# Performance work log

Measured on AMD Instinct MI355X. Metric: run time of the kernel, lower is better.

The kernel has to match this reference:

```python
import jax, jax.numpy as jnp
import numpy as np
import math

EPS = 1e-5


def _layernorm(x, gamma, beta):
    mu = jnp.mean(x, axis=-1, keepdims=True)
    var = jnp.var(x, axis=-1, keepdims=True)
    return (x - mu) * jax.lax.rsqrt(var + EPS) * gamma + beta


def _quantum_head(x, theta_rx):
    # RX(x_i) then RX(theta_i) on wire i == RX(x_i + theta_i); product state,
    # CNOT ring is a Z-basis permutation => <Z_j> = prod_{i in S_j} cos(a_i)
    # with S_j = {0..j} for j>=1 (chain of CNOT(i,i+1)) and S_0 = {1..7}
    # (final CNOT(7,0) makes b0 = b1^...^b7).
    c = jnp.cos(x + theta_rx)                       # (B,S,8)
    cp = jnp.cumprod(c, axis=-1)                    # prefix products c0..cj
    z0 = jnp.prod(c[..., 1:], axis=-1, keepdims=True)
    return jnp.concatenate([z0, cp[..., 1:]], axis=-1)  # (B,S,8)


def _quantum_ffn(x, theta_ry):
    # RX(x_i) |0>, then RY(theta_i), measure Z: <Z_i> = cos(theta_i) * cos(x_i)
    return jnp.cos(theta_ry) * jnp.cos(x)


def setup_inputs() -> dict:
    key = jax.random.key(0)
    ks = jax.random.split(key, 6)
    B, S, E, F = 16, 2048, 8, 512
    return {
        'x': jax.random.normal(ks[0], (B, S, E), jnp.float32),
        'theta_rx': jax.random.normal(ks[1], (E,), jnp.float32),
        'w_out': jax.random.normal(ks[2], (E, E), jnp.float32) / math.sqrt(E),
        'theta_ry': jax.random.normal(ks[3], (E,), jnp.float32),
        'w1': jax.random.normal(ks[4], (F, E), jnp.float32) / math.sqrt(E),
        'b1': jnp.zeros((F,), jnp.float32),
        'w2': jax.random.normal(ks[5], (E, F), jnp.float32) / math.sqrt(F),
        'b2': jnp.zeros((E,), jnp.float32),
        'gamma1': jnp.ones((E,), jnp.float32),
        'beta1': jnp.zeros((E,), jnp.float32),
        'gamma2': jnp.ones((E,), jnp.float32),
        'beta2': jnp.zeros((E,), jnp.float32),
    }


def reference(x, theta_rx, w_out, theta_ry, w1, b1, w2, b2,
              gamma1, beta1, gamma2, beta2):
    B, S, E = x.shape
    H = 2
    D = E // H
    # --- quantum multi-head attention (shared head => q == k == v) ---
    z = _quantum_head(x, theta_rx)                       # (B,S,E)
    qh = z.reshape(B, S, H, D).transpose(0, 2, 1, 3)     # (B,H,S,D)
    scores = jnp.einsum('bhqd,bhkd->bhqk', qh, qh) / math.sqrt(D)
    attn = jax.nn.softmax(scores, axis=-1)
    out = jnp.einsum('bhqk,bhkd->bhqd', attn, qh)        # (B,H,S,D)
    out = out.transpose(0, 2, 1, 3).reshape(B, S, E)
    attn_out = out @ w_out.T                             # out_proj, no bias
    x1 = _layernorm(x + attn_out, gamma1, beta1)
    # --- quantum feed-forward ---
    zf = _quantum_ffn(x1, theta_ry)                      # (B,S,E)
    h = zf @ w1.T + b1                                   # (B,S,F)
    ffn_out = jax.nn.relu(h) @ w2.T + b2                 # (B,S,E)
    return _layernorm(x1 + ffn_out, gamma2, beta2)
```

## Files before the change

### kernel.cpp

```cpp
#include <hip/hip_runtime.h>
#include <math.h>
#include <utility>

#define NB 16
#define NS 2048
#define NE 8
#define NH 2
#define NF 512
#define DEG 6
#define NMONO 210
#define KPB 64
#define NCHUNK 32
#define PHI_LD 66
#define QPB 128
#define LNEPS 1e-5f
#define PART_STRIDE (5 * NMONO)

typedef float f32x2 __attribute__((ext_vector_type(2)));
typedef _Float16 h2 __attribute__((ext_vector_type(2)));

#if defined(__has_builtin)
# if __has_builtin(__builtin_amdgcn_fdot2)
#  define FDOT2(a,b,c) __builtin_amdgcn_fdot2((a),(b),(c),false)
# endif
#endif
#ifndef FDOT2
static __device__ __forceinline__ float fdot2_sw(h2 a, h2 b, float c) {
    return c + (float)a.x * (float)b.x + (float)a.y * (float)b.y;
}
# define FDOT2(a,b,c) fdot2_sw((a),(b),(c))
#endif

constexpr float ACOEF_C[7] = {0.99994459f, 2.00308514f, 2.00174650f,
                              1.30890404f, 0.65803033f, 0.31441604f, 0.10241921f};

constexpr int mono_e(int idx) {
    int i = 0;
    for (int e0 = 0; e0 <= DEG; ++e0)
        for (int e1 = 0; e1 <= DEG - e0; ++e1)
            for (int e2 = 0; e2 <= DEG - e0 - e1; ++e2)
                for (int e3 = 0; e3 <= DEG - e0 - e1 - e2; ++e3) {
                    if (i == idx) return (e0 << 12) | (e1 << 8) | (e2 << 4) | e3;
                    ++i;
                }
    return 0;
}
constexpr float mfact(int n) { float r = 1.f; for (int i = 2; i <= n; ++i) r *= (float)i; return r; }
constexpr float mono_c(int idx) {
    const int E = mono_e(idx);
    const int e0 = E >> 12, e1 = (E >> 8) & 15, e2 = (E >> 4) & 15, e3 = E & 15;
    const int d = e0 + e1 + e2 + e3;
    return ACOEF_C[d] * (mfact(d) / (mfact(e0) * mfact(e1) * mfact(e2) * mfact(e3)));
}

template <int BEG, class F, int... Is>
__device__ __forceinline__ void sf_impl(F f, std::integer_sequence<int, Is...>) {
    (f(std::integral_constant<int, BEG + Is>{}), ...);
}
template <int BEG, int END, class F>
__device__ __forceinline__ void static_for(F f) {
    sf_impl<BEG>(f, std::make_integer_sequence<int, END - BEG>{});
}

template <int BEG, int END>
__device__ __forceinline__ void phi_body(_Float16* __restrict__ Phi, int lane,
                                         const float (&pw0)[7], const float (&pw1)[7],
                                         const float (&pw2)[7], const float (&pw3)[7]) {
    static_for<BEG, END>([&](auto Ic) {
        constexpr int idx = Ic.value;
        constexpr int E = mono_e(idx);
        constexpr float C = mono_c(idx);
        const float v = C * (pw0[E >> 12] * pw1[(E >> 8) & 15]) *
                            (pw2[(E >> 4) & 15] * pw3[E & 15]);
        Phi[idx * PHI_LD + lane] = (_Float16)v;
    });
}

__global__ __launch_bounds__(256, 4)
void k1_moments(const float* __restrict__ x, const float* __restrict__ theta_rx,
                float* __restrict__ ws) {
    __shared__ _Float16 Phi[NMONO * PHI_LD];
    __shared__ __align__(16) _Float16 kvh[KPB / 2][8];
    __shared__ float th_s[8];

    const int t = threadIdx.x, bid = blockIdx.x;
    const int kc = bid & 31, h = (bid >> 5) & 1, b = bid >> 6;

    if (t < 8) th_s[t] = theta_rx[t];
    __syncthreads();

    const int lane = t & 63, wq = t >> 6;
    {
        const float* xr = x + ((size_t)b * NS + kc * KPB + lane) * NE;
        const float4 v0 = *reinterpret_cast<const float4*>(xr);
        const float4 v1 = *reinterpret_cast<const float4*>(xr + 4);
        const float c0 = __cosf(v0.x + th_s[0]), c1 = __cosf(v0.y + th_s[1]);
        const float c2 = __cosf(v0.z + th_s[2]), c3 = __cosf(v0.w + th_s[3]);
        const float c4 = __cosf(v1.x + th_s[4]), c5 = __cosf(v1.y + th_s[5]);
        const float c6 = __cosf(v1.z + th_s[6]), c7 = __cosf(v1.w + th_s[7]);
        const float p1 = c0*c1, p2 = p1*c2, p3 = p2*c3, p4 = p3*c4;
        const float p5 = p4*c5, p6 = p5*c6, p7 = p6*c7;
        float k0, k1v, k2v, k3v;
        if (h == 0) {
            const float s6 = c7*c6, s5 = s6*c5, s4 = s5*c4, s3 = s4*c3, s2 = s3*c2;
            k0 = s2*c1; k1v = p1; k2v = p2; k3v = p3;
        } else {
            k0 = p4; k1v = p5; k2v = p6; k3v = p7;
        }
        if (t < 64) {
            const int j = t >> 1, par = t & 1;
            kvh[j][0 + par] = (_Float16)k0;  kvh[j][2 + par] = (_Float16)k1v;
            kvh[j][4 + par] = (_Float16)k2v; kvh[j][6 + par] = (_Float16)k3v;
        }
        float pw0[7], pw1[7], pw2[7], pw3[7];
        pw0[0] = pw1[0] = pw2[0] = pw3[0] = 1.f;
        #pragma unroll
        for (int i = 1; i <= DEG; ++i) {
            pw0[i] = pw0[i-1] * k0;  pw1[i] = pw1[i-1] * k1v;
            pw2[i] = pw2[i-1] * k2v; pw3[i] = pw3[i-1] * k3v;
        }
        switch (wq) {
            case 0: phi_body<0,   53 >(Phi, lane, pw0, pw1, pw2, pw3); break;
            case 1: phi_body<53,  106>(Phi, lane, pw0, pw1, pw2, pw3); break;
            case 2: phi_body<106, 159>(Phi, lane, pw0, pw1, pw2, pw3); break;
            default: phi_body<159, 210>(Phi, lane, pw0, pw1, pw2, pw3); break;
        }
    }
    __syncthreads();

    if (t < NMONO) {
        const h2 one2 = {(_Float16)1.f, (_Float16)1.f};
        float a0 = 0.f, a1 = 0.f, a2 = 0.f, a3 = 0.f, a4 = 0.f;
        #pragma unroll 8
        for (int j = 0; j < KPB / 2; ++j) {
            const h2 phi2 = *reinterpret_cast<const h2*>(&Phi[t * PHI_LD + 2 * j]);
            const float4 kv4 = *reinterpret_cast<const float4*>(&kvh[j][0]);
            const h2 kA = __builtin_bit_cast(h2, kv4.x);
            const h2 kB = __builtin_bit_cast(h2, kv4.y);
            const h2 kC = __builtin_bit_cast(h2, kv4.z);
            const h2 kD = __builtin_bit_cast(h2, kv4.w);
            a0 = FDOT2(phi2, kA, a0);
            a1 = FDOT2(phi2, kB, a1);
            a2 = FDOT2(phi2, kC, a2);
            a3 = FDOT2(phi2, kD, a3);
            a4 = FDOT2(phi2, one2, a4);
        }
        float* dst = ws + (size_t)bid * PART_STRIDE;
        dst[0 * NMONO + t] = a0;
        dst[1 * NMONO + t] = a1;
        dst[2 * NMONO + t] = a2;
        dst[3 * NMONO + t] = a3;
        dst[4 * NMONO + t] = a4;
    }
}

template <int BEG, int END>
__device__ __forceinline__ void p2_body1(const float4* __restrict__ Mn,
                                         const float* __restrict__ Md, int base,
                                         const float (&pw)[4][7],
                                         f32x2& a01, f32x2& a23, float& ad) {
    static_for<BEG, END>([&](auto Ic) {
        constexpr int idx = Ic.value;
        constexpr int E = mono_e(idx);
        constexpr int e0 = E >> 12, e1 = (E >> 8) & 15, e2 = (E >> 4) & 15, e3 = E & 15;
        const float4 mv = Mn[base + idx];
        const float  md = Md[base + idx];
        const float P = (pw[0][e0] * pw[1][e1]) * (pw[2][e2] * pw[3][e3]);
        a01 += P * (f32x2){mv.x, mv.y};
        a23 += P * (f32x2){mv.z, mv.w};
        ad  += P * md;
    });
}

__global__ __launch_bounds__(1024, 4)
void k2_main(const float* __restrict__ x, const float* __restrict__ theta_rx,
             const float* __restrict__ w_out, const float* __restrict__ theta_ry,
             const float* __restrict__ w1, const float* __restrict__ b1,
             const float* __restrict__ w2, const float* __restrict__ b2,
             const float* __restrict__ g1, const float* __restrict__ be1,
             const float* __restrict__ g2, const float* __restrict__ be2,
             const float* __restrict__ ws, float* __restrict__ out) {
    __shared__ float4 Mn_lds[2 * NMONO];
    __shared__ float  Md_lds[2 * NMONO];
    __shared__ float  z_c[8][QPB];
    __shared__ float  x1_c[8][QPB];
    __shared__ float  zf_c[8][QPB];
    __shared__ float  attn_c[8][QPB];
    __shared__ float  part_a[4][256][5];
    __shared__ float  w1_s[NF][NE];
    __shared__ float  w2t_s[NF][NE];
    __shared__ float  b1_s[NF];
    __shared__ float  wout_s[NE][NE];
    __shared__ float  th_s[8], cry_s[8], g1_s[8], be1_s[8], g2_s[8], be2_s[8], b2_s[8];

    const int t = threadIdx.x, bid = blockIdx.x;
    const int b  = (bid & 7) + 8 * ((bid >> 3) & 1);
    const int qc = bid >> 4;

    if (t < 2 * NMONO) {
        const int h = (t >= NMONO) ? 1 : 0;
        const int a = t - h * NMONO;
        const float* src = ws + (size_t)((b * 2 + h) * NCHUNK) * PART_STRIDE;
        float s0 = 0.f, s1 = 0.f, s2 = 0.f, s3 = 0.f, s4 = 0.f;
        #pragma unroll 4
        for (int kc = 0; kc < NCHUNK; ++kc) {
            const float* p = src + (size_t)kc * PART_STRIDE;
            s0 += p[0 * NMONO + a]; s1 += p[1 * NMONO + a];
            s2 += p[2 * NMONO + a]; s3 += p[3 * NMONO + a];
            s4 += p[4 * NMONO + a];
        }
        Mn_lds[t] = make_float4(s0, s1, s2, s3);
        Md_lds[t] = s4;
    }

    for (int i = t; i < NF * NE; i += 1024) {
        ((float*)w1_s)[i] = w1[i];
        const int e = i >> 9, f = i & (NF - 1);
        w2t_s[f][e] = w2[i];
    }
    if (t < NF) b1_s[t] = b1[t];
    if (t < NE * NE) ((float*)wout_s)[t] = w_out[t];
    if (t < 8) {
        th_s[t]  = theta_rx[t];
        cry_s[t] = __cosf(theta_ry[t]);
        g1_s[t]  = g1[t];  be1_s[t] = be1[t];
        g2_s[t]  = g2[t];  be2_s[t] = be2[t];
        b2_s[t]  = b2[t];
    }
    __syncthreads();

    if (t < QPB) {
        const float* xr = x + ((size_t)b * NS + qc * QPB + t) * NE;
        const float4 v0 = *reinterpret_cast<const float4*>(xr);
        const float4 v1 = *reinterpret_cast<const float4*>(xr + 4);
        const float c0 = __cosf(v0.x + th_s[0]), c1 = __cosf(v0.y + th_s[1]);
        const float c2 = __cosf(v0.z + th_s[2]), c3 = __cosf(v0.w + th_s[3]);
        const float c4 = __cosf(v1.x + th_s[4]), c5 = __cosf(v1.y + th_s[5]);
        const float c6 = __cosf(v1.z + th_s[6]), c7 = __cosf(v1.w + th_s[7]);
        const float p1 = c0*c1, p2 = p1*c2, p3 = p2*c3, p4 = p3*c4;
        const float p5 = p4*c5, p6 = p5*c6, p7 = p6*c7;
        const float s6 = c7*c6, s5 = s6*c5, s4 = s5*c4, s3 = s4*c3, s2 = s3*c2;
        z_c[0][t] = s2*c1; z_c[1][t] = p1; z_c[2][t] = p2; z_c[3][t] = p3;
        z_c[4][t] = p4;    z_c[5][t] = p5; z_c[6][t] = p6; z_c[7][t] = p7;
    }
    __syncthreads();

    {
        const int w = t >> 6, lane = t & 63;
        const int g = w & 3;
        const int h = (w >> 3) & 1;
        const int r = ((w >> 2) & 1) * 64 + lane;
        float pw[4][7];
        #pragma unroll
        for (int d = 0; d < 4; ++d) {
            const float u = z_c[h*4+d][r] * 0.25f;
            pw[d][0] = 1.f;
            #pragma unroll
            for (int i = 1; i <= DEG; ++i) pw[d][i] = pw[d][i-1] * u;
        }
        f32x2 a01 = {0.f,0.f}, a23 = {0.f,0.f};
        float ad = 0.f;
        const int base = h * NMONO;
        switch (g) {
            case 0: p2_body1<0,   53 >(Mn_lds, Md_lds, base, pw, a01, a23, ad); break;
            case 1: p2_body1<53,  106>(Mn_lds, Md_lds, base, pw, a01, a23, ad); break;
            case 2: p2_body1<106, 159>(Mn_lds, Md_lds, base, pw, a01, a23, ad); break;
            default: p2_body1<159, 210>(Mn_lds, Md_lds, base, pw, a01, a23, ad); break;
        }
        float* pa = &part_a[g][h * 128 + r][0];
        pa[0] = a01.x; pa[1] = a01.y; pa[2] = a23.x; pa[3] = a23.y; pa[4] = ad;
    }
    __syncthreads();

    if (t < 256) {
        const int h = t >> 7, r = t & 127;
        float n0 = 0.f, n1 = 0.f, n2 = 0.f, n3 = 0.f, dd = 0.f;
        #pragma unroll
        for (int g = 0; g < 4; ++g) {
            const float* pa = &part_a[g][t][0];
            n0 += pa[0]; n1 += pa[1]; n2 += pa[2]; n3 += pa[3]; dd += pa[4];
        }
        const float inv = 1.0f / dd;
        attn_c[h*4+0][r] = n0 * inv; attn_c[h*4+1][r] = n1 * inv;
        attn_c[h*4+2][r] = n2 * inv; attn_c[h*4+3][r] = n3 * inv;
    }
    __syncthreads();

    if (t < QPB) {
        float av[NE];
        #pragma unroll
        for (int e = 0; e < NE; ++e) av[e] = attn_c[e][t];
        float y[NE];
        #pragma unroll
        for (int e = 0; e < NE; ++e) {
            float acc = 0.f;
            #pragma unroll
            for (int k = 0; k < NE; ++k) acc += av[k] * wout_s[e][k];
            y[e] = acc;
        }
        const float* xr = x + ((size_t)b * NS + qc * QPB + t) * NE;
        const float4 xv0 = *reinterpret_cast<const float4*>(xr);
        const float4 xv1 = *reinterpret_cast<const float4*>(xr + 4);
        float t1[NE];
        t1[0] = xv0.x + y[0]; t1[1] = xv0.y + y[1]; t1[2] = xv0.z + y[2]; t1[3] = xv0.w + y[3];
        t1[4] = xv1.x + y[4]; t1[5] = xv1.y + y[5]; t1[6] = xv1.z + y[6]; t1[7] = xv1.w + y[7];
        float mu = 0.f;
        #pragma unroll
        for (int e = 0; e < NE; ++e) mu += t1[e];
        mu *= 0.125f;
        float var = 0.f;
        #pragma unroll
        for (int e = 0; e < NE; ++e) { const float d = t1[e] - mu; var += d * d; }
        var *= 0.125f;
        const float inv1 = rsqrtf(var + LNEPS);
        #pragma unroll
        for (int e = 0; e < NE; ++e) {
            const float x1e = (t1[e] - mu) * inv1 * g1_s[e] + be1_s[e];
            x1_c[e][t] = x1e;
            zf_c[e][t] = cry_s[e] * __cosf(x1e);
        }
    }
    __syncthreads();

    {
        const int r = t >> 3, sub = t & 7;
        float zf[NE];
        #pragma unroll
        for (int e = 0; e < NE; ++e) zf[e] = zf_c[e][r];
        f32x2 a01 = {0.f,0.f}, a23 = {0.f,0.f}, a45 = {0.f,0.f}, a67 = {0.f,0.f};
        #pragma unroll 8
        for (int i = 0; i < 64; ++i) {
            const int f = sub + (i << 3);
            const float4 wa = *reinterpret_cast<const float4*>(&w1_s[f][0]);
            const float4 wb = *reinterpret_cast<const float4*>(&w1_s[f][4]);
            float hv = b1_s[f] + zf[0]*wa.x + zf[1]*wa.y + zf[2]*wa.z + zf[3]*wa.w
                               + zf[4]*wb.x + zf[5]*wb.y + zf[6]*wb.z + zf[7]*wb.w;
            hv = fmaxf(hv, 0.f);
            const float4 ua = *reinterpret_cast<const float4*>(&w2t_s[f][0]);
            const float4 ub = *reinterpret_cast<const float4*>(&w2t_s[f][4]);
            a01 += hv * (f32x2){ua.x, ua.y};
            a23 += hv * (f32x2){ua.z, ua.w};
            a45 += hv * (f32x2){ub.x, ub.y};
            a67 += hv * (f32x2){ub.z, ub.w};
        }
        float acc[NE] = {a01.x, a01.y, a23.x, a23.y, a45.x, a45.y, a67.x, a67.y};
        #pragma unroll
        for (int m = 1; m < 8; m <<= 1) {
            #pragma unroll
            for (int e = 0; e < NE; ++e) acc[e] += __shfl_xor(acc[e], m, 64);
        }
        float t2[NE];
        #pragma unroll
        for (int e = 0; e < NE; ++e) t2[e] = x1_c[e][r] + acc[e] + b2_s[e];
        float mu = 0.f;
        #pragma unroll
        for (int e = 0; e < NE; ++e) mu += t2[e];
        mu *= 0.125f;
        float var = 0.f;
        #pragma unroll
        for (int e = 0; e < NE; ++e) { const float d = t2[e] - mu; var += d * d; }
        var *= 0.125f;
        const float inv2 = rsqrtf(var + LNEPS);
        out[((size_t)b * NS + qc * QPB + r) * NE + sub] =
            (t2[sub] - mu) * inv2 * g2_s[sub] + be2_s[sub];
    }
}

extern "C" void kernel_launch(void* const* d_in, const int* in_sizes, int n_in,
                              void* d_out, int out_size, void* d_ws, size_t ws_size,
                              hipStream_t stream) {
    const float* x        = (const float*)d_in[0];
    const float* theta_rx = (const float*)d_in[1];
    const float* w_out    = (const float*)d_in[2];
    const float* theta_ry = (const float*)d_in[3];
    const float* w1       = (const float*)d_in[4];
    const float* b1       = (const float*)d_in[5];
    const float* w2       = (const float*)d_in[6];
    const float* b2       = (const float*)d_in[7];
    const float* g1       = (const float*)d_in[8];
    const float* be1      = (const float*)d_in[9];
    const float* g2       = (const float*)d_in[10];
    const float* be2      = (const float*)d_in[11];
    float* out = (float*)d_out;
    float* ws  = (float*)d_ws;

    k1_moments<<<dim3(NB * NH * NCHUNK), dim3(256), 0, stream>>>(x, theta_rx, ws);
    k2_main<<<dim3(NB * (NS / QPB)), dim3(1024), 0, stream>>>(
        x, theta_rx, w_out, theta_ry, w1, b1, w2, b2, g1, be1, g2, be2, ws, out);
}
```

Before: 33.03 us.

## Use fp16 dot2 and packed fp16 FFN math, merge attention-norm stage across threads

Stores w1 and transposed w2 in shared memory as fp16, computes the FFN hidden layer with fdot2 instructions, and accumulates the second matmul in packed fp16 (including the shuffle reduction). It also merges the attention normalisation and out-projection/LayerNorm1 stages into one stage that uses all 1024 threads with 8-lane shuffles, removing a barrier and the attn_c buffer. The goal is fewer ALU ops, less LDS traffic and shorter serial phases. The cost is reduced precision: accumulating 512 products in fp16 may exceed tolerance.

```diff
diff --git a/kernel.cpp b/kernel.cpp
--- a/kernel.cpp
+++ b/kernel.cpp
@@ -185,10 +185,9 @@
     __shared__ float  z_c[8][QPB];
     __shared__ float  x1_c[8][QPB];
     __shared__ float  zf_c[8][QPB];
-    __shared__ float  attn_c[8][QPB];
     __shared__ float  part_a[4][256][5];
-    __shared__ float  w1_s[NF][NE];
-    __shared__ float  w2t_s[NF][NE];
+    __shared__ __align__(16) _Float16 w1h[NF][8];
+    __shared__ __align__(16) _Float16 w2th[NF][8];
     __shared__ float  b1_s[NF];
     __shared__ float  wout_s[NE][NE];
     __shared__ float  th_s[8], cry_s[8], g1_s[8], be1_s[8], g2_s[8], be2_s[8], b2_s[8];
@@ -214,9 +213,9 @@
     }
 
     for (int i = t; i < NF * NE; i += 1024) {
-        ((float*)w1_s)[i] = w1[i];
+        ((_Float16*)w1h)[i] = (_Float16)w1[i];
         const int e = i >> 9, f = i & (NF - 1);
-        w2t_s[f][e] = w2[i];
+        w2th[f][e] = (_Float16)w2[i];
     }
     if (t < NF) b1_s[t] = b1[t];
     if (t < NE * NE) ((float*)wout_s)[t] = w_out[t];
@@ -272,86 +271,84 @@
     }
     __syncthreads();
 
-    if (t < 256) {
-        const int h = t >> 7, r = t & 127;
-        float n0 = 0.f, n1 = 0.f, n2 = 0.f, n3 = 0.f, dd = 0.f;
-        #pragma unroll
-        for (int g = 0; g < 4; ++g) {
-            const float* pa = &part_a[g][t][0];
-            n0 += pa[0]; n1 += pa[1]; n2 += pa[2]; n3 += pa[3]; dd += pa[4];
-        }
-        const float inv = 1.0f / dd;
-        attn_c[h*4+0][r] = n0 * inv; attn_c[h*4+1][r] = n1 * inv;
-        attn_c[h*4+2][r] = n2 * inv; attn_c[h*4+3][r] = n3 * inv;
-    }
-    __syncthreads();
-
-    if (t < QPB) {
+    {
+        const int r = t >> 3, sub = t & 7;
         float av[NE];
         #pragma unroll
-        for (int e = 0; e < NE; ++e) av[e] = attn_c[e][t];
-        float y[NE];
-        #pragma unroll
-        for (int e = 0; e < NE; ++e) {
-            float acc = 0.f;
+        for (int h = 0; h < 2; ++h) {
+            float n0 = 0.f, n1 = 0.f, n2 = 0.f, n3 = 0.f, dd = 0.f;
             #pragma unroll
-            for (int k = 0; k < NE; ++k) acc += av[k] * wout_s[e][k];
-            y[e] = acc;
-        }
-        const float* xr = x + ((size_t)b * NS + qc * QPB + t) * NE;
-        const float4 xv0 = *reinterpret_cast<const float4*>(xr);
-        const float4 xv1 = *reinterpret_cast<const float4*>(xr + 4);
-        float t1[NE];
-        t1[0] = xv0.x + y[0]; t1[1] = xv0.y + y[1]; t1[2] = xv0.z + y[2]; t1[3] = xv0.w + y[3];
-        t1[4] = xv1.x + y[4]; t1[5] = xv1.y + y[5]; t1[6] = xv1.z + y[6]; t1[7] = xv1.w + y[7];
-        float mu = 0.f;
-        #pragma unroll
-        for (int e = 0; e < NE; ++e) mu += t1[e];
+            for (int g = 0; g < 4; ++g) {
+                const float* pa = &part_a[g][h * 128 + r][0];
+                n0 += pa[0]; n1 += pa[1]; n2 += pa[2]; n3 += pa[3]; dd += pa[4];
+            }
+            const float inv = 1.0f / dd;
+            av[h*4+0] = n0 * inv; av[h*4+1] = n1 * inv;
+            av[h*4+2] = n2 * inv; av[h*4+3] = n3 * inv;
+        }
+        float y = 0.f;
+        #pragma unroll
+        for (int k = 0; k < NE; ++k) y += av[k] * wout_s[sub][k];
+        const float xv = x[((size_t)b * NS + qc * QPB + r) * NE + sub];
+        const float t1 = xv + y;
+        float mu = t1;
+        mu += __shfl_xor(mu, 1, 64); mu += __shfl_xor(mu, 2, 64); mu += __shfl_xor(mu, 4, 64);
         mu *= 0.125f;
-        float var = 0.f;
-        #pragma unroll
-        for (int e = 0; e < NE; ++e) { const float d = t1[e] - mu; var += d * d; }
+        const float d = t1 - mu;
+        float var = d * d;
+        var += __shfl_xor(var, 1, 64); var += __shfl_xor(var, 2, 64); var += __shfl_xor(var, 4, 64);
         var *= 0.125f;
         const float inv1 = rsqrtf(var + LNEPS);
-        #pragma unroll
-        for (int e = 0; e < NE; ++e) {
-            const float x1e = (t1[e] - mu) * inv1 * g1_s[e] + be1_s[e];
-            x1_c[e][t] = x1e;
-            zf_c[e][t] = cry_s[e] * __cosf(x1e);
-        }
+        const float x1e = d * inv1 * g1_s[sub] + be1_s[sub];
+        x1_c[sub][r] = x1e;
+        zf_c[sub][r] = cry_s[sub] * __cosf(x1e);
     }
     __syncthreads();
 
     {
         const int r = t >> 3, sub = t & 7;
-        float zf[NE];
-        #pragma unroll
-        for (int e = 0; e < NE; ++e) zf[e] = zf_c[e][r];
-        f32x2 a01 = {0.f,0.f}, a23 = {0.f,0.f}, a45 = {0.f,0.f}, a67 = {0.f,0.f};
+        float zfl[NE];
+        #pragma unroll
+        for (int e = 0; e < NE; ++e) zfl[e] = zf_c[e][r];
+        const h2 zp0 = {(_Float16)zfl[0], (_Float16)zfl[1]};
+        const h2 zp1 = {(_Float16)zfl[2], (_Float16)zfl[3]};
+        const h2 zp2 = {(_Float16)zfl[4], (_Float16)zfl[5]};
+        const h2 zp3 = {(_Float16)zfl[6], (_Float16)zfl[7]};
+        h2 acc0 = {(_Float16)0.f, (_Float16)0.f}, acc1 = acc0, acc2 = acc0, acc3 = acc0;
         #pragma unroll 8
         for (int i = 0; i < 64; ++i) {
             const int f = sub + (i << 3);
-            const float4 wa = *reinterpret_cast<const float4*>(&w1_s[f][0]);
-            const float4 wb = *reinterpret_cast<const float4*>(&w1_s[f][4]);
-            float hv = b1_s[f] + zf[0]*wa.x + zf[1]*wa.y + zf[2]*wa.z + zf[3]*wa.w
-                               + zf[4]*wb.x + zf[5]*wb.y + zf[6]*wb.z + zf[7]*wb.w;
+            const float4 wv = *reinterpret_cast<const float4*>(&w1h[f][0]);
+            float hv = b1_s[f];
+            hv = FDOT2(zp0, __builtin_bit_cast(h2, wv.x), hv);
+            hv = FDOT2(zp1, __builtin_bit_cast(h2, wv.y), hv);
+            hv = FDOT2(zp2, __builtin_bit_cast(h2, wv.z), hv);
+            hv = FDOT2(zp3, __builtin_bit_cast(h2, wv.w), hv);
             hv = fmaxf(hv, 0.f);
-            const float4 ua = *reinterpret_cast<const float4*>(&w2t_s[f][0]);
-            const float4 ub = *reinterpret_cast<const float4*>(&w2t_s[f][4]);
-            a01 += hv * (f32x2){ua.x, ua.y};
-            a23 += hv * (f32x2){ua.z, ua.w};
-            a45 += hv * (f32x2){ub.x, ub.y};
-            a67 += hv * (f32x2){ub.z, ub.w};
-        }
-        float acc[NE] = {a01.x, a01.y, a23.x, a23.y, a45.x, a45.y, a67.x, a67.y};
+            const _Float16 hh = (_Float16)hv;
+            const h2 hv2 = {hh, hh};
+            const float4 uv = *reinterpret_cast<const float4*>(&w2th[f][0]);
+            acc0 += hv2 * __builtin_bit_cast(h2, uv.x);
+            acc1 += hv2 * __builtin_bit_cast(h2, uv.y);
+            acc2 += hv2 * __builtin_bit_cast(h2, uv.z);
+            acc3 += hv2 * __builtin_bit_cast(h2, uv.w);
+        }
         #pragma unroll
         for (int m = 1; m < 8; m <<= 1) {
-            #pragma unroll
-            for (int e = 0; e < NE; ++e) acc[e] += __shfl_xor(acc[e], m, 64);
+            acc0 += __builtin_bit_cast(h2, __shfl_xor(__builtin_bit_cast(float, acc0), m, 64));
+            acc1 += __builtin_bit_cast(h2, __shfl_xor(__builtin_bit_cast(float, acc1), m, 64));
+            acc2 += __builtin_bit_cast(h2, __shfl_xor(__builtin_bit_cast(float, acc2), m, 64));
+            acc3 += __builtin_bit_cast(h2, __shfl_xor(__builtin_bit_cast(float, acc3), m, 64));
         }
         float t2[NE];
-        #pragma unroll
-        for (int e = 0; e < NE; ++e) t2[e] = x1_c[e][r] + acc[e] + b2_s[e];
+        t2[0] = x1_c[0][r] + (float)acc0.x + b2_s[0];
+        t2[1] = x1_c[1][r] + (float)acc0.y + b2_s[1];
+        t2[2] = x1_c[2][r] + (float)acc1.x + b2_s[2];
+        t2[3] = x1_c[3][r] + (float)acc1.y + b2_s[3];
+        t2[4] = x1_c[4][r] + (float)acc2.x + b2_s[4];
+        t2[5] = x1_c[5][r] + (float)acc2.y + b2_s[5];
+        t2[6] = x1_c[6][r] + (float)acc3.x + b2_s[6];
+        t2[7] = x1_c[7][r] + (float)acc3.y + b2_s[7];
         float mu = 0.f;
         #pragma unroll
         for (int e = 0; e < NE; ++e) mu += t2[e];
```

Measured after the change: 29.54 us. -10.6%, faster.
